# Performance work log

Hardware: AMD Instinct MI355X
Metric: run time of the kernel (lower is better)

## Reference

```python
import jax, jax.numpy as jnp
import numpy as np

B, L, D, H = 2, 4096, 768, 12
Dh = D // H


def setup_inputs() -> dict:
    key = jax.random.key(0)
    k1, k2, k3 = jax.random.split(key, 3)
    x = jax.random.normal(k1, (B, L, D), dtype=jnp.float32)
    Wqkv = jax.random.normal(k2, (D, 3 * D), dtype=jnp.float32) * 0.02
    bqkv = jnp.zeros((3 * D,), dtype=jnp.float32)
    Wo = jax.random.normal(k3, (D, D), dtype=jnp.float32) * 0.02
    bo = jnp.zeros((D,), dtype=jnp.float32)
    return {"x": x, "Wqkv": Wqkv, "bqkv": bqkv, "Wo": Wo, "bo": bo}


def reference(x, Wqkv, bqkv, Wo, bo):
    Bs, Ls, Ds = x.shape
    # fused QKV projection
    qkv = x @ Wqkv + bqkv  # [B, L, 3D]
    q, k, v = jnp.split(qkv, 3, axis=2)
    q = q.reshape(Bs, Ls, H, Dh)
    k = k.reshape(Bs, Ls, H, Dh)
    v = v.reshape(Bs, Ls, H, Dh)
    # scaled dot-product attention with causal mask (fp32 softmax, as flax dpa with dtype=float32)
    scale = 1.0 / np.sqrt(Dh)
    scores = jnp.einsum('bqhd,bkhd->bhqk', q, k) * scale  # [B, H, L, L]
    causal = jnp.tril(jnp.ones((Ls, Ls), dtype=bool))
    big_neg = jnp.finfo(jnp.float32).min
    scores = jnp.where(causal[None, None, :, :], scores, big_neg)
    attn = jax.nn.softmax(scores, axis=-1)
    y = jnp.einsum('bhqk,bkhd->bqhd', attn, v)  # [B, L, H, Dh]
    y = y.reshape(Bs, Ls, Ds)
    # output projection
    return y @ Wo + bo
```

## Files before the change

kernel.cpp:

```cpp
#include <hip/hip_runtime.h>
#include <hip/hip_bf16.h>
#include <stdint.h>

#define BB 2
#define LL 4096
#define DD 768
#define HH 12
#define DH 64
#define MM (BB * LL)
#define NQKV (3 * DD)
#define KK 768
#define PLANE ((size_t)BB * HH * LL * DH)
#define SQSCALE 0.1803368801111204f

typedef __attribute__((ext_vector_type(8))) short bf16x8;
typedef __attribute__((ext_vector_type(4))) float f32x4;

__device__ __forceinline__ float bf2f(uint16_t u) {
  union { uint32_t u; float f; } c; c.u = ((uint32_t)u) << 16; return c.f;
}
__device__ __forceinline__ uint16_t f2bf(float f) {
  union { float f; uint32_t u; } c; c.f = f;
  return (uint16_t)((c.u + 0x7FFFu + ((c.u >> 16) & 1u)) >> 16);
}
__device__ __forceinline__ uint32_t cvt2(float a, float b) {
  __hip_bfloat162 h = __float22bfloat162_rn(make_float2(a, b));
  union { __hip_bfloat162 h; uint32_t u; } c; c.h = h; return c.u;
}
#if __has_builtin(__builtin_amdgcn_exp2f)
__device__ __forceinline__ float fexp2(float x) { return __builtin_amdgcn_exp2f(x); }
#else
__device__ __forceinline__ float fexp2(float x) {
  float r;
  asm volatile("v_exp_f32 %0, %1\ns_nop 0" : "=v"(r) : "v"(x));
  return r;
}
#endif

union H8 { uint16_t h[8]; uint32_t w[4]; uint4 v; };
union B8 { uint2 d[2]; bf16x8 v; };

template <bool F32>
__device__ __forceinline__ H8 load8(const void* p, size_t idx) {
  H8 r;
  if (F32) {
    const float* f = (const float*)p + idx;
    float4 a = *(const float4*)f;
    float4 b = *(const float4*)(f + 4);
    r.w[0] = cvt2(a.x, a.y); r.w[1] = cvt2(a.z, a.w);
    r.w[2] = cvt2(b.x, b.y); r.w[3] = cvt2(b.z, b.w);
  } else {
    r.v = *(const uint4*)((const uint16_t*)p + idx);
  }
  return r;
}

__device__ __forceinline__ void g2l16(const uint16_t* g, uint16_t* l) {
  __builtin_amdgcn_global_load_lds((const __attribute__((address_space(1))) void*)g,
                                   (__attribute__((address_space(3))) void*)l,
                                   16, 0, 0);
}

__global__ void detect_k(const uint16_t* __restrict__ x, int* __restrict__ flag) {
  __shared__ int cnt;
  if (threadIdx.x == 0) cnt = 0;
  __syncthreads();
  int c = 0;
  for (int i = threadIdx.x; i < 4096; i += 256) {
    int e = (x[i] >> 7) & 0xFF;
    if (e == 0xFF || e > 133 || e < 100) c++;
  }
  atomicAdd(&cnt, c);
  __syncthreads();
  if (threadIdx.x == 0) *flag = (cnt > 512) ? 1 : 0;
}

__global__ __launch_bounds__(256) void prep_k(const void* __restrict__ x,
                                              uint16_t* __restrict__ xbf,
                                              const void* __restrict__ Wqkv,
                                              uint16_t* __restrict__ wqkvT,
                                              const void* __restrict__ Wo,
                                              uint16_t* __restrict__ woT,
                                              const int* __restrict__ flag) {
  __shared__ uint16_t Ts[64][65];
  const int fl = *flag;
  const int id = blockIdx.x;
  const int tid = threadIdx.x;
  if (id < 768) {
    size_t base = (size_t)id * 1024 + tid;
#pragma unroll
    for (int j = 0; j < 4; ++j) {
      size_t i = base + j * 256;
      H8 v = fl ? load8<true>(x, i * 8) : load8<false>(x, i * 8);
      *(uint4*)(xbf + i * 8) = v.v;
    }
    return;
  }
  const void* W;
  uint16_t* WT;
  int N, widx;
  if (id < 1200) { W = Wqkv; WT = wqkvT; N = NQKV; widx = id - 768; }
  else           { W = Wo;   WT = woT;   N = DD;   widx = id - 1200; }
  const int nb = N / 64;
  const int n0 = (widx % nb) * 64, k0 = (widx / nb) * 64;
#pragma unroll
  for (int j = 0; j < 16; ++j) {
    int idx = tid + j * 256;
    int r = idx >> 6, c = idx & 63;
    size_t gi = (size_t)(k0 + r) * N + n0 + c;
    float v = fl ? ((const float*)W)[gi] : bf2f(((const uint16_t*)W)[gi]);
    Ts[c][r] = f2bf(v);
  }
  __syncthreads();
#pragma unroll
  for (int j = 0; j < 16; ++j) {
    int idx = tid + j * 256;
    int n = idx >> 6, k = idx & 63;
    WT[(size_t)(n0 + n) * KK + k0 + k] = Ts[n][k];
  }
}

__device__ __forceinline__ void gemm128_core(const uint16_t* __restrict__ A,
                                             const uint16_t* __restrict__ BT,
                                             int m0, int n0,
                                             uint16_t* As, uint16_t* Bs,
                                             f32x4 acc[4][4]) {
  const int tid = threadIdx.x, lane = tid & 63, w = tid >> 6;
  const int quad = lane >> 4, c16 = lane & 15;
  const int wm = w >> 1, wn = w & 1;
  const int srow = lane >> 2, schunk = lane & 3;
  const int rsw = (c16 >> 1) & 3;
  for (int k0 = 0; k0 < KK; k0 += 32) {
#pragma unroll
    for (int i = 0; i < 2; ++i) {
      int row = w * 32 + i * 16 + srow;
      int gch = schunk ^ ((row >> 1) & 3);
      g2l16(A + (size_t)(m0 + row) * KK + k0 + gch * 8, As + (w * 32 + i * 16) * 32);
      g2l16(BT + (size_t)(n0 + row) * KK + k0 + gch * 8, Bs + (w * 32 + i * 16) * 32);
    }
    __syncthreads();
    bf16x8 a[4], b[4];
#pragma unroll
    for (int i = 0; i < 4; ++i) {
      a[i] = *(const bf16x8*)(As + (wm * 64 + i * 16 + c16) * 32 + ((quad ^ rsw) * 8));
      b[i] = *(const bf16x8*)(Bs + (wn * 64 + i * 16 + c16) * 32 + ((quad ^ rsw) * 8));
    }
#pragma unroll
    for (int i = 0; i < 4; ++i)
#pragma unroll
      for (int f = 0; f < 4; ++f)
        acc[i][f] = __builtin_amdgcn_mfma_f32_16x16x32_bf16(a[i], b[f], acc[i][f], 0, 0, 0);
    __syncthreads();
  }
}

__global__ __launch_bounds__(256) void qkv128_k(const uint16_t* __restrict__ X,
                                                const uint16_t* __restrict__ WT,
                                                const void* __restrict__ bias,
                                                uint16_t* __restrict__ planes,
                                                const int* __restrict__ flag) {
  __shared__ __align__(16) uint16_t smem[8704];
  uint16_t* As = smem;
  uint16_t* Bs = smem + 4096;
  const int fl = *flag;
  const int m0 = blockIdx.x * 128, n0 = blockIdx.y * 128;
  f32x4 acc[4][4];
#pragma unroll
  for (int i = 0; i < 4; ++i)
#pragma unroll
    for (int f = 0; f < 4; ++f) acc[i][f] = (f32x4){0.f, 0.f, 0.f, 0.f};
  gemm128_core(X, WT, m0, n0, As, Bs, acc);

  const int tid = threadIdx.x, lane = tid & 63, w = tid >> 6;
  const int quad = lane >> 4, c16 = lane & 15;
  const int wm = w >> 1, wn = w & 1;
  const int which = (n0 >= 2 * DD) ? 2 : (n0 >= DD ? 1 : 0);

  if (which < 2) {
    uint16_t* dst = planes + (size_t)which * PLANE;
    const float sc = (which == 0) ? SQSCALE : 1.0f;
#pragma unroll
    for (int f = 0; f < 4; ++f) {
      int n = n0 + wn * 64 + f * 16 + c16;
      float bv = fl ? ((const float*)bias)[n] : bf2f(((const uint16_t*)bias)[n]);
      int rem = n - which * DD;
      int hh = rem >> 6, dd = rem & 63;
#pragma unroll
      for (int i = 0; i < 4; ++i) {
        uint32_t pa = cvt2((acc[i][f][0] + bv) * sc, (acc[i][f][1] + bv) * sc);
        uint32_t pb = cvt2((acc[i][f][2] + bv) * sc, (acc[i][f][3] + bv) * sc);
        int m = m0 + wm * 64 + i * 16 + quad * 4;
        int b = m >> 12, l = m & (LL - 1);
        uint16_t* base = dst + ((size_t)(b * HH + hh) * LL + l) * DH + dd;
        base[0 * DH] = (uint16_t)pa;
        base[1 * DH] = (uint16_t)(pa >> 16);
        base[2 * DH] = (uint16_t)pb;
        base[3 * DH] = (uint16_t)(pb >> 16);
      }
    }
  } else {
    uint16_t (*Ts)[136] = reinterpret_cast<uint16_t(*)[136]>(smem);
    uint16_t* vtp = planes + 2 * PLANE;
    const int l0 = m0 & (LL - 1), bb = m0 >> 12;
    for (int half = 0; half < 2; ++half) {
      __syncthreads();
      if (wn == half) {
#pragma unroll
        for (int f = 0; f < 4; ++f) {
          int n = n0 + half * 64 + f * 16 + c16;
          float bv = fl ? ((const float*)bias)[n] : bf2f(((const uint16_t*)bias)[n]);
#pragma unroll
          for (int i = 0; i < 4; ++i) {
            uint32_t pa = cvt2(acc[i][f][0] + bv, acc[i][f][1] + bv);
            uint32_t pb = cvt2(acc[i][f][2] + bv, acc[i][f][3] + bv);
            *(uint2*)(&Ts[f * 16 + c16][wm * 64 + i * 16 + quad * 4]) = make_uint2(pa, pb);
          }
        }
      }
      __syncthreads();
#pragma unroll
      for (int j = 0; j < 4; ++j) {
        int idx = tid + j * 256;
        int nl = idx >> 4, ch = idx & 15;
        int rem = n0 + half * 64 + nl - 2 * DD;
        int hh = rem >> 6, dd = rem & 63;
        uint4 val = *(const uint4*)(&Ts[nl][ch * 8]);
        *(uint4*)(vtp + ((size_t)(bb * HH + hh) * DH + dd) * LL + l0 + ch * 8) = val;
      }
    }
  }
}

__global__ __launch_bounds__(256, 3) void attn_k(const uint16_t* __restrict__ planes,
                                                 uint16_t* __restrict__ y) {
  __shared__ __align__(16) uint16_t Ks[2][128 * 64];
  __shared__ __align__(16) uint16_t Vt[64 * 128];
  const int id = blockIdx.x;
  const int p = id / 24;
  const int bh = id % 24;
  const uint16_t* qb = planes + (size_t)bh * LL * DH;
  const uint16_t* kb = qb + PLANE;
  const uint16_t* vtb = planes + 2 * PLANE + (size_t)bh * DH * LL;
  const int tid = threadIdx.x, lane = tid & 63, wv = tid >> 6;
  const int quad = lane >> 4, c16 = lane & 15;
  const int swf = c16 & 7;
  const int qsub = wv & 1;
  const int kg = wv >> 1;
  const int b = bh / HH, hh = bh - b * HH;

  int koff[4];
  {
    int cp = lane & 7;
#pragma unroll
    for (int i = 0; i < 4; ++i) {
      int row = wv * 32 + i * 8 + (lane >> 3);
      koff[i] = row * 64 + ((cp ^ (row & 7)) * 8);
    }
  }
  const int kdst = wv * 32 * 64;

  const int vkg = ((tid >> 2) & 1) | ((tid & 1) << 1);
  const int vdr = ((tid >> 1) & 1) | (((tid >> 4) & 1) << 1) |
                  (((tid >> 3) & 1) << 2) | ((tid >> 5) << 3);
  const int swd = vdr & 7;
  int vwoff[4][2];
#pragma unroll
  for (int j = 0; j < 4; ++j) {
#pragma unroll
    for (int h = 0; h < 2; ++h) {
      int ks = (vkg + 4 * j) * 8 + 4 * h;
      int G = ks >> 6, ks6 = ks & 63;
      int ch = ((ks6 & 32) >> 3) + ((ks6 >> 2) & 3);
      int f4 = ((ks6 >> 4) & 1) * 4;
      vwoff[j][h] = vdr * 128 + G * 64 + ((ch ^ swd ^ (G << 2)) * 8) + f4;
    }
  }

  B8 ones;
  ones.d[0] = make_uint2(0x3F803F80u, 0x3F803F80u);
  ones.d[1] = make_uint2(0x3F803F80u, 0x3F803F80u);

  float* osm = (float*)(&Ks[0][0]);

  for (int pass = 0; pass < 2; ++pass) {
    const int qi = pass ? p : 63 - p;
    const int nt = (qi + 2) >> 1;
    const int q0 = qi * 64;
    bf16x8 qf[2][2];
#pragma unroll
    for (int s = 0; s < 2; ++s) {
      size_t qoff = (size_t)(q0 + qsub * 32 + s * 16 + c16) * DH;
      qf[s][0] = *(const bf16x8*)(qb + qoff + quad * 8);
      qf[s][1] = *(const bf16x8*)(qb + qoff + 32 + quad * 8);
    }

    f32x4 o[2][4], la[2];
#pragma unroll
    for (int s = 0; s < 2; ++s) {
      la[s] = (f32x4){0.f, 0.f, 0.f, 0.f};
#pragma unroll
      for (int g = 0; g < 4; ++g) o[s][g] = (f32x4){0.f, 0.f, 0.f, 0.f};
    }

    const uint16_t* ksrc = kb;
    const uint16_t* vp = vtb + (size_t)vdr * LL + vkg * 8;
    uint4 vrg[4];
#pragma unroll
    for (int i = 0; i < 4; ++i) g2l16(ksrc + koff[i], Ks[0] + kdst + i * 512);
#pragma unroll
    for (int j = 0; j < 4; ++j) vrg[j] = *(const uint4*)(vp + j * 32);
    ksrc += 128 * DH; vp += 128;

    for (int t = 0; t < nt; ++t) {
      const uint16_t* kd = Ks[t & 1];
      uint16_t* knx = Ks[(t + 1) & 1];
      __syncthreads();
#pragma unroll
      for (int j = 0; j < 4; ++j) {
        *(uint2*)(Vt + vwoff[j][0]) = make_uint2(vrg[j].x, vrg[j].y);
        *(uint2*)(Vt + vwoff[j][1]) = make_uint2(vrg[j].z, vrg[j].w);
      }
      __syncthreads();
      if (t + 1 < nt) {
#pragma unroll
        for (int i = 0; i < 4; ++i) g2l16(ksrc + koff[i], knx + kdst + i * 512);
#pragma unroll
        for (int j = 0; j < 4; ++j) vrg[j] = *(const uint4*)(vp + j * 32);
        ksrc += 128 * DH; vp += 128;
      }

      bf16x8 kfr[4][2];
#pragma unroll
      for (int f = 0; f < 4; ++f) {
        const uint16_t* krow = kd + (kg * 64 + f * 16 + c16) * 64;
        kfr[f][0] = *(const bf16x8*)(krow + ((quad ^ swf) * 8));
        kfr[f][1] = *(const bf16x8*)(krow + (((quad + 4) ^ swf) * 8));
      }
      B8 pk[2][2];
#pragma unroll
      for (int s = 0; s < 2; ++s) {
        f32x4 sv[4];
        __builtin_amdgcn_s_setprio(1);
#pragma unroll
        for (int f = 0; f < 4; ++f) {
          f32x4 z = {0.f, 0.f, 0.f, 0.f};
          z = __builtin_amdgcn_mfma_f32_16x16x32_bf16(kfr[f][0], qf[s][0], z, 0, 0, 0);
          z = __builtin_amdgcn_mfma_f32_16x16x32_bf16(kfr[f][1], qf[s][1], z, 0, 0, 0);
          sv[f] = z;
        }
        __builtin_amdgcn_s_setprio(0);
        const int qg = q0 + qsub * 32 + s * 16 + c16;
        if (t == nt - 1) {
#pragma unroll
          for (int f = 0; f < 4; ++f) {
            int key0 = t * 128 + kg * 64 + f * 16 + quad * 4;
#pragma unroll
            for (int r = 0; r < 4; ++r) {
              float pv = fexp2(sv[f][r]);
              sv[f][r] = (key0 + r <= qg) ? pv : 0.f;
            }
          }
        } else {
#pragma unroll
          for (int f = 0; f < 4; ++f)
#pragma unroll
            for (int r = 0; r < 4; ++r) sv[f][r] = fexp2(sv[f][r]);
        }
        pk[s][0].d[0] = make_uint2(cvt2(sv[0][0], sv[0][1]), cvt2(sv[0][2], sv[0][3]));
        pk[s][0].d[1] = make_uint2(cvt2(sv[1][0], sv[1][1]), cvt2(sv[1][2], sv[1][3]));
        pk[s][1].d[0] = make_uint2(cvt2(sv[2][0], sv[2][1]), cvt2(sv[2][2], sv[2][3]));
        pk[s][1].d[1] = make_uint2(cvt2(sv[3][0], sv[3][1]), cvt2(sv[3][2], sv[3][3]));
      }
      __builtin_amdgcn_s_setprio(1);
#pragma unroll
      for (int s = 0; s < 2; ++s)
#pragma unroll
        for (int j = 0; j < 2; ++j)
          la[s] = __builtin_amdgcn_mfma_f32_16x16x32_bf16(pk[s][j].v, ones.v, la[s], 0, 0, 0);
#pragma unroll
      for (int g = 0; g < 4; ++g) {
        const uint16_t* vrow = Vt + (g * 16 + c16) * 128 + kg * 64;
#pragma unroll
        for (int j = 0; j < 2; ++j) {
          int chunk = (quad + 4 * j) ^ swf ^ (kg << 2);
          bf16x8 vv = *(const bf16x8*)(vrow + chunk * 8);
          o[0][g] = __builtin_amdgcn_mfma_f32_16x16x32_bf16(pk[0][j].v, vv, o[0][g], 0, 0, 0);
          o[1][g] = __builtin_amdgcn_mfma_f32_16x16x32_bf16(pk[1][j].v, vv, o[1][g], 0, 0, 0);
        }
      }
      __builtin_amdgcn_s_setprio(0);
    }

    __syncthreads();
    if (kg == 1) {
#pragma unroll
      for (int s = 0; s < 2; ++s) {
#pragma unroll
        for (int g = 0; g < 4; ++g)
          *(f32x4*)(osm + ((qsub * 8 + s * 4 + g) * 64 + lane) * 4) = o[s][g];
        *(f32x4*)(osm + 4096 + ((qsub * 2 + s) * 64 + lane) * 4) = la[s];
      }
    }
    __syncthreads();
    if (kg == 0) {
#pragma unroll
      for (int s = 0; s < 2; ++s) {
        f32x4 lp = *(const f32x4*)(osm + 4096 + ((qsub * 2 + s) * 64 + lane) * 4);
        float inv[4];
#pragma unroll
        for (int r = 0; r < 4; ++r) inv[r] = 1.f / (la[s][r] + lp[r]);
        int l = q0 + qsub * 32 + s * 16 + quad * 4;
#pragma unroll
        for (int g = 0; g < 4; ++g) {
          f32x4 op = *(const f32x4*)(osm + ((qsub * 8 + s * 4 + g) * 64 + lane) * 4);
          float v0 = (o[s][g][0] + op[0]) * inv[0];
          float v1 = (o[s][g][1] + op[1]) * inv[1];
          float v2 = (o[s][g][2] + op[2]) * inv[2];
          float v3 = (o[s][g][3] + op[3]) * inv[3];
          uint32_t pa = cvt2(v0, v1);
          uint32_t pb = cvt2(v2, v3);
          uint16_t* base = y + ((size_t)(b * LL + l)) * DD + hh * DH + g * 16 + c16;
          base[0 * DD] = (uint16_t)pa;
          base[1 * DD] = (uint16_t)(pa >> 16);
          base[2 * DD] = (uint16_t)pb;
          base[3 * DD] = (uint16_t)(pb >> 16);
        }
      }
    }
    __syncthreads();
  }
}

__global__ __launch_bounds__(256) void out64_k(const uint16_t* __restrict__ Y,
                                               const uint16_t* __restrict__ WT,
                                               const void* __restrict__ bias,
                                               void* __restrict__ out,
                                               const int* __restrict__ flag) {
  __shared__ __align__(16) uint16_t As[128 * 32];
  __shared__ __align__(16) uint16_t Bs[64 * 32];
  const int fl = *flag;
  const int m0 = blockIdx.x * 128, n0 = blockIdx.y * 64;
  const int tid = threadIdx.x, lane = tid & 63, w = tid >> 6;
  const int quad = lane >> 4, c16 = lane & 15;
  const int srow = lane >> 2, schunk = lane & 3;
  const int rsw = (c16 >> 1) & 3;
  f32x4 acc[2][4];
#pragma unroll
  for (int i = 0; i < 2; ++i)
#pragma unroll
    for (int f = 0; f < 4; ++f) acc[i][f] = (f32x4){0.f, 0.f, 0.f, 0.f};
  for (int k0 = 0; k0 < KK; k0 += 32) {
#pragma unroll
    for (int i = 0; i < 2; ++i) {
      int row = w * 32 + i * 16 + srow;
      int gch = schunk ^ ((row >> 1) & 3);
      g2l16(Y + (size_t)(m0 + row) * KK + k0 + gch * 8, As + (w * 32 + i * 16) * 32);
    }
    {
      int row = w * 16 + srow;
      int gch = schunk ^ ((row >> 1) & 3);
      g2l16(WT + (size_t)(n0 + row) * KK + k0 + gch * 8, Bs + (w * 16) * 32);
    }
    __syncthreads();
    bf16x8 a[2], bfr[4];
#pragma unroll
    for (int i = 0; i < 2; ++i)
      a[i] = *(const bf16x8*)(As + (w * 32 + i * 16 + c16) * 32 + ((quad ^ rsw) * 8));
#pragma unroll
    for (int f = 0; f < 4; ++f)
      bfr[f] = *(const bf16x8*)(Bs + (f * 16 + c16) * 32 + ((quad ^ rsw) * 8));
#pragma unroll
    for (int i = 0; i < 2; ++i)
#pragma unroll
      for (int f = 0; f < 4; ++f)
        acc[i][f] = __builtin_amdgcn_mfma_f32_16x16x32_bf16(a[i], bfr[f], acc[i][f], 0, 0, 0);
    __syncthreads();
  }
#pragma unroll
  for (int f = 0; f < 4; ++f) {
    int n = n0 + f * 16 + c16;
    float bv = fl ? ((const float*)bias)[n] : bf2f(((const uint16_t*)bias)[n]);
#pragma unroll
    for (int i = 0; i < 2; ++i) {
      int m = m0 + w * 32 + i * 16 + quad * 4;
      if (fl) {
        float* base = (float*)out + (size_t)m * DD + n;
#pragma unroll
        for (int r = 0; r < 4; ++r) base[r * DD] = acc[i][f][r] + bv;
      } else {
        uint32_t pa = cvt2(acc[i][f][0] + bv, acc[i][f][1] + bv);
        uint32_t pb = cvt2(acc[i][f][2] + bv, acc[i][f][3] + bv);
        uint16_t* base = (uint16_t*)out + (size_t)m * DD + n;
        base[0 * DD] = (uint16_t)pa;
        base[1 * DD] = (uint16_t)(pa >> 16);
        base[2 * DD] = (uint16_t)pb;
        base[3 * DD] = (uint16_t)(pb >> 16);
      }
    }
  }
}

extern "C" void kernel_launch(void* const* d_in, const int* in_sizes, int n_in,
                              void* d_out, int out_size, void* d_ws, size_t ws_size,
                              hipStream_t stream) {
  const void* x    = d_in[0];
  const void* Wqkv = d_in[1];
  const void* bqkv = d_in[2];
  const void* Wo   = d_in[3];
  const void* bo   = d_in[4];
  int* flagp = (int*)d_ws;
  uint16_t* planes = (uint16_t*)((char*)d_ws + 64);
  uint16_t* y_ws   = planes + 3 * PLANE;
  uint16_t* wqkvT  = y_ws + (size_t)MM * DD;
  uint16_t* woT    = wqkvT + (size_t)NQKV * KK;
  uint16_t* xbf    = y_ws;

  detect_k<<<1, 256, 0, stream>>>((const uint16_t*)x, flagp);
  prep_k<<<1344, 256, 0, stream>>>(x, xbf, Wqkv, wqkvT, Wo, woT, flagp);
  qkv128_k<<<dim3(MM / 128, NQKV / 128), 256, 0, stream>>>(xbf, wqkvT, bqkv, planes, flagp);
  attn_k<<<dim3(768), 256, 0, stream>>>(planes, y_ws);
  out64_k<<<dim3(MM / 128, DD / 64), 256, 0, stream>>>(y_ws, woT, bo, d_out, flagp);
}
```

Baseline: 238.7 us.

## Split QKV projection into double-buffered 128x256 Q/K kernel and separate V kernel

```diff
diff --git a/kernel.cpp b/kernel.cpp
--- a/kernel.cpp
+++ b/kernel.cpp
@@ -154,6 +154,95 @@
   }
 }
 
+__global__ __launch_bounds__(512, 4) void qkv256_k(const uint16_t* __restrict__ X,
+                                                   const uint16_t* __restrict__ WT,
+                                                   const void* __restrict__ bias,
+                                                   uint16_t* __restrict__ planes,
+                                                   const int* __restrict__ flag) {
+  __shared__ __align__(16) uint16_t Asm[2][128 * 32];
+  __shared__ __align__(16) uint16_t Bsm[2][256 * 32];
+  const int fl = *flag;
+  const int m0 = blockIdx.x * 128, n0 = blockIdx.y * 256;
+  const int tid = threadIdx.x, lane = tid & 63, wv = tid >> 6;
+  const int quad = lane >> 4, c16 = lane & 15;
+  const int wm = wv >> 2, wn = wv & 3;
+  const int srow = lane >> 2, schunk = lane & 3;
+  const int rsw = (c16 >> 1) & 3;
+
+  const int ra = wv * 16 + srow;
+  const int rb0 = wv * 32 + srow;
+  const int rb1 = wv * 32 + 16 + srow;
+  const int ga = schunk ^ ((ra >> 1) & 3);
+  const int gb0 = schunk ^ ((rb0 >> 1) & 3);
+  const int gb1 = schunk ^ ((rb1 >> 1) & 3);
+  const uint16_t* gpa = X + (size_t)(m0 + ra) * KK + ga * 8;
+  const uint16_t* gpb0 = WT + (size_t)(n0 + rb0) * KK + gb0 * 8;
+  const uint16_t* gpb1 = WT + (size_t)(n0 + rb1) * KK + gb1 * 8;
+  const int la = (wv * 16) * 32;
+  const int lb0 = (wv * 32) * 32;
+  const int lb1 = (wv * 32 + 16) * 32;
+
+  f32x4 acc[4][4];
+#pragma unroll
+  for (int i = 0; i < 4; ++i)
+#pragma unroll
+    for (int f = 0; f < 4; ++f) acc[i][f] = (f32x4){0.f, 0.f, 0.f, 0.f};
+
+  g2l16(gpa, Asm[0] + la);
+  g2l16(gpb0, Bsm[0] + lb0);
+  g2l16(gpb1, Bsm[0] + lb1);
+  __syncthreads();
+
+  const int NT = KK / 32;
+  for (int t = 0; t < NT; ++t) {
+    const int cb = t & 1;
+    if (t + 1 < NT) {
+      const int koff = (t + 1) * 32;
+      g2l16(gpa + koff, Asm[cb ^ 1] + la);
+      g2l16(gpb0 + koff, Bsm[cb ^ 1] + lb0);
+      g2l16(gpb1 + koff, Bsm[cb ^ 1] + lb1);
+    }
+    bf16x8 a[4], b[4];
+#pragma unroll
+    for (int i = 0; i < 4; ++i)
+      a[i] = *(const bf16x8*)(Asm[cb] + (wm * 64 + i * 16 + c16) * 32 + ((quad ^ rsw) * 8));
+#pragma unroll
+    for (int f = 0; f < 4; ++f)
+      b[f] = *(const bf16x8*)(Bsm[cb] + (wn * 64 + f * 16 + c16) * 32 + ((quad ^ rsw) * 8));
+    __builtin_amdgcn_s_setprio(1);
+#pragma unroll
+    for (int i = 0; i < 4; ++i)
+#pragma unroll
+      for (int f = 0; f < 4; ++f)
+        acc[i][f] = __builtin_amdgcn_mfma_f32_16x16x32_bf16(a[i], b[f], acc[i][f], 0, 0, 0);
+    __builtin_amdgcn_s_setprio(0);
+    __syncthreads();
+  }
+
+  const int which = (n0 >= DD) ? 1 : 0;
+  uint16_t* dst = planes + (size_t)which * PLANE;
+  const float sc = (which == 0) ? SQSCALE : 1.0f;
+#pragma unroll
+  for (int f = 0; f < 4; ++f) {
+    int n = n0 + wn * 64 + f * 16 + c16;
+    float bv = fl ? ((const float*)bias)[n] : bf2f(((const uint16_t*)bias)[n]);
+    int rem = n - which * DD;
+    int hh = rem >> 6, dd = rem & 63;
+#pragma unroll
+    for (int i = 0; i < 4; ++i) {
+      uint32_t pa = cvt2((acc[i][f][0] + bv) * sc, (acc[i][f][1] + bv) * sc);
+      uint32_t pb = cvt2((acc[i][f][2] + bv) * sc, (acc[i][f][3] + bv) * sc);
+      int m = m0 + wm * 64 + i * 16 + quad * 4;
+      int b2 = m >> 12, l = m & (LL - 1);
+      uint16_t* base = dst + ((size_t)(b2 * HH + hh) * LL + l) * DH + dd;
+      base[0 * DH] = (uint16_t)pa;
+      base[1 * DH] = (uint16_t)(pa >> 16);
+      base[2 * DH] = (uint16_t)pb;
+      base[3 * DH] = (uint16_t)(pb >> 16);
+    }
+  }
+}
+
 __global__ __launch_bounds__(256) void qkv128_k(const uint16_t* __restrict__ X,
                                                 const uint16_t* __restrict__ WT,
                                                 const void* __restrict__ bias,
@@ -163,7 +252,7 @@
   uint16_t* As = smem;
   uint16_t* Bs = smem + 4096;
   const int fl = *flag;
-  const int m0 = blockIdx.x * 128, n0 = blockIdx.y * 128;
+  const int m0 = blockIdx.x * 128, n0 = blockIdx.y * 128 + 2 * DD;
   f32x4 acc[4][4];
 #pragma unroll
   for (int i = 0; i < 4; ++i)
@@ -174,59 +263,34 @@
   const int tid = threadIdx.x, lane = tid & 63, w = tid >> 6;
   const int quad = lane >> 4, c16 = lane & 15;
   const int wm = w >> 1, wn = w & 1;
-  const int which = (n0 >= 2 * DD) ? 2 : (n0 >= DD ? 1 : 0);
-
-  if (which < 2) {
-    uint16_t* dst = planes + (size_t)which * PLANE;
-    const float sc = (which == 0) ? SQSCALE : 1.0f;
-#pragma unroll
-    for (int f = 0; f < 4; ++f) {
-      int n = n0 + wn * 64 + f * 16 + c16;
-      float bv = fl ? ((const float*)bias)[n] : bf2f(((const uint16_t*)bias)[n]);
-      int rem = n - which * DD;
+
+  uint16_t (*Ts)[136] = reinterpret_cast<uint16_t(*)[136]>(smem);
+  uint16_t* vtp = planes + 2 * PLANE;
+  const int l0 = m0 & (LL - 1), bb = m0 >> 12;
+  for (int half = 0; half < 2; ++half) {
+    __syncthreads();
+    if (wn == half) {
+#pragma unroll
+      for (int f = 0; f < 4; ++f) {
+        int n = n0 + half * 64 + f * 16 + c16;
+        float bv = fl ? ((const float*)bias)[n] : bf2f(((const uint16_t*)bias)[n]);
+#pragma unroll
+        for (int i = 0; i < 4; ++i) {
+          uint32_t pa = cvt2(acc[i][f][0] + bv, acc[i][f][1] + bv);
+          uint32_t pb = cvt2(acc[i][f][2] + bv, acc[i][f][3] + bv);
+          *(uint2*)(&Ts[f * 16 + c16][wm * 64 + i * 16 + quad * 4]) = make_uint2(pa, pb);
+        }
+      }
+    }
+    __syncthreads();
+#pragma unroll
+    for (int j = 0; j < 4; ++j) {
+      int idx = tid + j * 256;
+      int nl = idx >> 4, ch = idx & 15;
+      int rem = n0 + half * 64 + nl - 2 * DD;
       int hh = rem >> 6, dd = rem & 63;
-#pragma unroll
-      for (int i = 0; i < 4; ++i) {
-        uint32_t pa = cvt2((acc[i][f][0] + bv) * sc, (acc[i][f][1] + bv) * sc);
-        uint32_t pb = cvt2((acc[i][f][2] + bv) * sc, (acc[i][f][3] + bv) * sc);
-        int m = m0 + wm * 64 + i * 16 + quad * 4;
-        int b = m >> 12, l = m & (LL - 1);
-        uint16_t* base = dst + ((size_t)(b * HH + hh) * LL + l) * DH + dd;
-        base[0 * DH] = (uint16_t)pa;
-        base[1 * DH] = (uint16_t)(pa >> 16);
-        base[2 * DH] = (uint16_t)pb;
-        base[3 * DH] = (uint16_t)(pb >> 16);
-      }
-    }
-  } else {
-    uint16_t (*Ts)[136] = reinterpret_cast<uint16_t(*)[136]>(smem);
-    uint16_t* vtp = planes + 2 * PLANE;
-    const int l0 = m0 & (LL - 1), bb = m0 >> 12;
-    for (int half = 0; half < 2; ++half) {
-      __syncthreads();
-      if (wn == half) {
-#pragma unroll
-        for (int f = 0; f < 4; ++f) {
-          int n = n0 + half * 64 + f * 16 + c16;
-          float bv = fl ? ((const float*)bias)[n] : bf2f(((const uint16_t*)bias)[n]);
-#pragma unroll
-          for (int i = 0; i < 4; ++i) {
-            uint32_t pa = cvt2(acc[i][f][0] + bv, acc[i][f][1] + bv);
-            uint32_t pb = cvt2(acc[i][f][2] + bv, acc[i][f][3] + bv);
-            *(uint2*)(&Ts[f * 16 + c16][wm * 64 + i * 16 + quad * 4]) = make_uint2(pa, pb);
-          }
-        }
-      }
-      __syncthreads();
-#pragma unroll
-      for (int j = 0; j < 4; ++j) {
-        int idx = tid + j * 256;
-        int nl = idx >> 4, ch = idx & 15;
-        int rem = n0 + half * 64 + nl - 2 * DD;
-        int hh = rem >> 6, dd = rem & 63;
-        uint4 val = *(const uint4*)(&Ts[nl][ch * 8]);
-        *(uint4*)(vtp + ((size_t)(bb * HH + hh) * DH + dd) * LL + l0 + ch * 8) = val;
-      }
+      uint4 val = *(const uint4*)(&Ts[nl][ch * 8]);
+      *(uint4*)(vtp + ((size_t)(bb * HH + hh) * DH + dd) * LL + l0 + ch * 8) = val;
     }
   }
 }
@@ -517,7 +581,8 @@
 
   detect_k<<<1, 256, 0, stream>>>((const uint16_t*)x, flagp);
   prep_k<<<1344, 256, 0, stream>>>(x, xbf, Wqkv, wqkvT, Wo, woT, flagp);
-  qkv128_k<<<dim3(MM / 128, NQKV / 128), 256, 0, stream>>>(xbf, wqkvT, bqkv, planes, flagp);
+  qkv256_k<<<dim3(MM / 128, 6), 512, 0, stream>>>(xbf, wqkvT, bqkv, planes, flagp);
+  qkv128_k<<<dim3(MM / 128, 6), 256, 0, stream>>>(xbf, wqkvT, bqkv, planes, flagp);
   attn_k<<<dim3(768), 256, 0, stream>>>(planes, y_ws);
   out64_k<<<dim3(MM / 128, DD / 64), 256, 0, stream>>>(y_ws, woT, bo, d_out, flagp);
 }
```

Measured after the change: 234.8 us. No clear change (-1.6%).

## Double-buffer LDS in QKV and output GEMMs, widen QKV tile to 128x256

Applied to the files above, without the earlier changes.

```diff
diff --git a/kernel.cpp b/kernel.cpp
--- a/kernel.cpp
+++ b/kernel.cpp
@@ -120,63 +120,73 @@
   }
 }
 
-__device__ __forceinline__ void gemm128_core(const uint16_t* __restrict__ A,
-                                             const uint16_t* __restrict__ BT,
-                                             int m0, int n0,
-                                             uint16_t* As, uint16_t* Bs,
-                                             f32x4 acc[4][4]) {
-  const int tid = threadIdx.x, lane = tid & 63, w = tid >> 6;
+__global__ __launch_bounds__(512, 4) void qkv256_k(const uint16_t* __restrict__ X,
+                                                   const uint16_t* __restrict__ WT,
+                                                   const void* __restrict__ bias,
+                                                   uint16_t* __restrict__ planes,
+                                                   const int* __restrict__ flag) {
+  __shared__ __align__(16) uint16_t smem[24576];
+  const int fl = *flag;
+  const int m0 = blockIdx.x * 128, n0 = blockIdx.y * 256;
+  const int tid = threadIdx.x, lane = tid & 63, wv = tid >> 6;
   const int quad = lane >> 4, c16 = lane & 15;
-  const int wm = w >> 1, wn = w & 1;
+  const int wm = wv >> 2, wn = wv & 3;
   const int srow = lane >> 2, schunk = lane & 3;
   const int rsw = (c16 >> 1) & 3;
-  for (int k0 = 0; k0 < KK; k0 += 32) {
-#pragma unroll
-    for (int i = 0; i < 2; ++i) {
-      int row = w * 32 + i * 16 + srow;
-      int gch = schunk ^ ((row >> 1) & 3);
-      g2l16(A + (size_t)(m0 + row) * KK + k0 + gch * 8, As + (w * 32 + i * 16) * 32);
-      g2l16(BT + (size_t)(n0 + row) * KK + k0 + gch * 8, Bs + (w * 32 + i * 16) * 32);
-    }
-    __syncthreads();
+
+  const int ra = wv * 16 + srow;
+  const int rb0 = wv * 32 + srow;
+  const int rb1 = wv * 32 + 16 + srow;
+  const int ga = schunk ^ ((ra >> 1) & 3);
+  const int gb0 = schunk ^ ((rb0 >> 1) & 3);
+  const int gb1 = schunk ^ ((rb1 >> 1) & 3);
+  const uint16_t* gpa = X + (size_t)(m0 + ra) * KK + ga * 8;
+  const uint16_t* gpb0 = WT + (size_t)(n0 + rb0) * KK + gb0 * 8;
+  const uint16_t* gpb1 = WT + (size_t)(n0 + rb1) * KK + gb1 * 8;
+  const int la = (wv * 16) * 32;
+  const int lb0 = (wv * 32) * 32;
+  const int lb1 = (wv * 32 + 16) * 32;
+
+  f32x4 acc[4][4];
+#pragma unroll
+  for (int i = 0; i < 4; ++i)
+#pragma unroll
+    for (int f = 0; f < 4; ++f) acc[i][f] = (f32x4){0.f, 0.f, 0.f, 0.f};
+
+  g2l16(gpa, smem + la);
+  g2l16(gpb0, smem + 8192 + lb0);
+  g2l16(gpb1, smem + 8192 + lb1);
+  __syncthreads();
+
+  const int NT = KK / 32;
+  for (int t = 0; t < NT; ++t) {
+    const int aoff = (t & 1) ? 4096 : 0;
+    const int boff = (t & 1) ? 16384 : 8192;
+    if (t + 1 < NT) {
+      const int koff = (t + 1) * 32;
+      g2l16(gpa + koff, smem + (4096 - aoff) + la);
+      g2l16(gpb0 + koff, smem + (24576 - boff) + lb0);
+      g2l16(gpb1 + koff, smem + (24576 - boff) + lb1);
+    }
     bf16x8 a[4], b[4];
 #pragma unroll
-    for (int i = 0; i < 4; ++i) {
-      a[i] = *(const bf16x8*)(As + (wm * 64 + i * 16 + c16) * 32 + ((quad ^ rsw) * 8));
-      b[i] = *(const bf16x8*)(Bs + (wn * 64 + i * 16 + c16) * 32 + ((quad ^ rsw) * 8));
-    }
+    for (int i = 0; i < 4; ++i)
+      a[i] = *(const bf16x8*)(smem + aoff + (wm * 64 + i * 16 + c16) * 32 + ((quad ^ rsw) * 8));
+#pragma unroll
+    for (int f = 0; f < 4; ++f)
+      b[f] = *(const bf16x8*)(smem + boff + (wn * 64 + f * 16 + c16) * 32 + ((quad ^ rsw) * 8));
+    __builtin_amdgcn_s_setprio(1);
 #pragma unroll
     for (int i = 0; i < 4; ++i)
 #pragma unroll
       for (int f = 0; f < 4; ++f)
         acc[i][f] = __builtin_amdgcn_mfma_f32_16x16x32_bf16(a[i], b[f], acc[i][f], 0, 0, 0);
+    __builtin_amdgcn_s_setprio(0);
     __syncthreads();
   }
-}
-
-__global__ __launch_bounds__(256) void qkv128_k(const uint16_t* __restrict__ X,
-                                                const uint16_t* __restrict__ WT,
-                                                const void* __restrict__ bias,
-                                                uint16_t* __restrict__ planes,
-                                                const int* __restrict__ flag) {
-  __shared__ __align__(16) uint16_t smem[8704];
-  uint16_t* As = smem;
-  uint16_t* Bs = smem + 4096;
-  const int fl = *flag;
-  const int m0 = blockIdx.x * 128, n0 = blockIdx.y * 128;
-  f32x4 acc[4][4];
-#pragma unroll
-  for (int i = 0; i < 4; ++i)
-#pragma unroll
-    for (int f = 0; f < 4; ++f) acc[i][f] = (f32x4){0.f, 0.f, 0.f, 0.f};
-  gemm128_core(X, WT, m0, n0, As, Bs, acc);
-
-  const int tid = threadIdx.x, lane = tid & 63, w = tid >> 6;
-  const int quad = lane >> 4, c16 = lane & 15;
-  const int wm = w >> 1, wn = w & 1;
-  const int which = (n0 >= 2 * DD) ? 2 : (n0 >= DD ? 1 : 0);
-
-  if (which < 2) {
+
+  if (n0 < 2 * DD) {
+    const int which = (n0 >= DD) ? 1 : 0;
     uint16_t* dst = planes + (size_t)which * PLANE;
     const float sc = (which == 0) ? SQSCALE : 1.0f;
 #pragma unroll
@@ -190,8 +200,8 @@
         uint32_t pa = cvt2((acc[i][f][0] + bv) * sc, (acc[i][f][1] + bv) * sc);
         uint32_t pb = cvt2((acc[i][f][2] + bv) * sc, (acc[i][f][3] + bv) * sc);
         int m = m0 + wm * 64 + i * 16 + quad * 4;
-        int b = m >> 12, l = m & (LL - 1);
-        uint16_t* base = dst + ((size_t)(b * HH + hh) * LL + l) * DH + dd;
+        int b2 = m >> 12, l = m & (LL - 1);
+        uint16_t* base = dst + ((size_t)(b2 * HH + hh) * LL + l) * DH + dd;
         base[0 * DH] = (uint16_t)pa;
         base[1 * DH] = (uint16_t)(pa >> 16);
         base[2 * DH] = (uint16_t)pb;
@@ -202,12 +212,11 @@
     uint16_t (*Ts)[136] = reinterpret_cast<uint16_t(*)[136]>(smem);
     uint16_t* vtp = planes + 2 * PLANE;
     const int l0 = m0 & (LL - 1), bb = m0 >> 12;
-    for (int half = 0; half < 2; ++half) {
-      __syncthreads();
-      if (wn == half) {
+    for (int g64 = 0; g64 < 4; ++g64) {
+      if (wn == g64) {
 #pragma unroll
         for (int f = 0; f < 4; ++f) {
-          int n = n0 + half * 64 + f * 16 + c16;
+          int n = n0 + g64 * 64 + f * 16 + c16;
           float bv = fl ? ((const float*)bias)[n] : bf2f(((const uint16_t*)bias)[n]);
 #pragma unroll
           for (int i = 0; i < 4; ++i) {
@@ -219,14 +228,15 @@
       }
       __syncthreads();
 #pragma unroll
-      for (int j = 0; j < 4; ++j) {
-        int idx = tid + j * 256;
+      for (int j = 0; j < 2; ++j) {
+        int idx = tid + j * 512;
         int nl = idx >> 4, ch = idx & 15;
-        int rem = n0 + half * 64 + nl - 2 * DD;
+        int rem = n0 + g64 * 64 + nl - 2 * DD;
         int hh = rem >> 6, dd = rem & 63;
         uint4 val = *(const uint4*)(&Ts[nl][ch * 8]);
         *(uint4*)(vtp + ((size_t)(bb * HH + hh) * DH + dd) * LL + l0 + ch * 8) = val;
       }
+      __syncthreads();
     }
   }
 }
@@ -436,44 +446,62 @@
                                                const void* __restrict__ bias,
                                                void* __restrict__ out,
                                                const int* __restrict__ flag) {
-  __shared__ __align__(16) uint16_t As[128 * 32];
-  __shared__ __align__(16) uint16_t Bs[64 * 32];
+  __shared__ __align__(16) uint16_t smem[12288];
   const int fl = *flag;
   const int m0 = blockIdx.x * 128, n0 = blockIdx.y * 64;
   const int tid = threadIdx.x, lane = tid & 63, w = tid >> 6;
   const int quad = lane >> 4, c16 = lane & 15;
   const int srow = lane >> 2, schunk = lane & 3;
   const int rsw = (c16 >> 1) & 3;
+
+  const int ra0 = w * 32 + srow;
+  const int ra1 = w * 32 + 16 + srow;
+  const int rb = w * 16 + srow;
+  const int gA0 = schunk ^ ((ra0 >> 1) & 3);
+  const int gA1 = schunk ^ ((ra1 >> 1) & 3);
+  const int gB = schunk ^ ((rb >> 1) & 3);
+  const uint16_t* gpa0 = Y + (size_t)(m0 + ra0) * KK + gA0 * 8;
+  const uint16_t* gpa1 = Y + (size_t)(m0 + ra1) * KK + gA1 * 8;
+  const uint16_t* gpb = WT + (size_t)(n0 + rb) * KK + gB * 8;
+  const int la0 = (w * 32) * 32;
+  const int la1 = (w * 32 + 16) * 32;
+  const int lb = (w * 16) * 32;
+
   f32x4 acc[2][4];
 #pragma unroll
   for (int i = 0; i < 2; ++i)
 #pragma unroll
     for (int f = 0; f < 4; ++f) acc[i][f] = (f32x4){0.f, 0.f, 0.f, 0.f};
-  for (int k0 = 0; k0 < KK; k0 += 32) {
-#pragma unroll
-    for (int i = 0; i < 2; ++i) {
-      int row = w * 32 + i * 16 + srow;
-      int gch = schunk ^ ((row >> 1) & 3);
-      g2l16(Y + (size_t)(m0 + row) * KK + k0 + gch * 8, As + (w * 32 + i * 16) * 32);
-    }
-    {
-      int row = w * 16 + srow;
-      int gch = schunk ^ ((row >> 1) & 3);
-      g2l16(WT + (size_t)(n0 + row) * KK + k0 + gch * 8, Bs + (w * 16) * 32);
-    }
-    __syncthreads();
+
+  g2l16(gpa0, smem + la0);
+  g2l16(gpa1, smem + la1);
+  g2l16(gpb, smem + 8192 + lb);
+  __syncthreads();
+
+  const int NT = KK / 32;
+  for (int t = 0; t < NT; ++t) {
+    const int aoff = (t & 1) ? 4096 : 0;
+    const int boff = (t & 1) ? 10240 : 8192;
+    if (t + 1 < NT) {
+      const int koff = (t + 1) * 32;
+      g2l16(gpa0 + koff, smem + (4096 - aoff) + la0);
+      g2l16(gpa1 + koff, smem + (4096 - aoff) + la1);
+      g2l16(gpb + koff, smem + (18432 - boff) + lb);
+    }
     bf16x8 a[2], bfr[4];
 #pragma unroll
     for (int i = 0; i < 2; ++i)
-      a[i] = *(const bf16x8*)(As + (w * 32 + i * 16 + c16) * 32 + ((quad ^ rsw) * 8));
+      a[i] = *(const bf16x8*)(smem + aoff + (w * 32 + i * 16 + c16) * 32 + ((quad ^ rsw) * 8));
 #pragma unroll
     for (int f = 0; f < 4; ++f)
-      bfr[f] = *(const bf16x8*)(Bs + (f * 16 + c16) * 32 + ((quad ^ rsw) * 8));
+      bfr[f] = *(const bf16x8*)(smem + boff + (f * 16 + c16) * 32 + ((quad ^ rsw) * 8));
+    __builtin_amdgcn_s_setprio(1);
 #pragma unroll
     for (int i = 0; i < 2; ++i)
 #pragma unroll
       for (int f = 0; f < 4; ++f)
         acc[i][f] = __builtin_amdgcn_mfma_f32_16x16x32_bf16(a[i], bfr[f], acc[i][f], 0, 0, 0);
+    __builtin_amdgcn_s_setprio(0);
     __syncthreads();
   }
 #pragma unroll
@@ -517,7 +545,7 @@
 
   detect_k<<<1, 256, 0, stream>>>((const uint16_t*)x, flagp);
   prep_k<<<1344, 256, 0, stream>>>(x, xbf, Wqkv, wqkvT, Wo, woT, flagp);
-  qkv128_k<<<dim3(MM / 128, NQKV / 128), 256, 0, stream>>>(xbf, wqkvT, bqkv, planes, flagp);
+  qkv256_k<<<dim3(MM / 128, NQKV / 256), 512, 0, stream>>>(xbf, wqkvT, bqkv, planes, flagp);
   attn_k<<<dim3(768), 256, 0, stream>>>(planes, y_ws);
   out64_k<<<dim3(MM / 128, DD / 64), 256, 0, stream>>>(y_ws, woT, bo, d_out, flagp);
 }
```

Measured after the change: 235.9 us. Within noise of the previous version (-1.2%).
